# Optimization experiments

Measured on AMD Instinct MI355X. Metric: run time of the kernel, lower is better.

## Reference

```python
import jax, jax.numpy as jnp
import numpy as np
from jax import lax

WINDOW_SIZE = 11
SIGMA = 1.5
IMG_RANGE = 2.0
MS_WEIGHTS = np.array([0.0448, 0.2856, 0.3001, 0.2363, 0.1333], dtype=np.float32)


def _gauss_window(k=WINDOW_SIZE, sigma=SIGMA):
    x = np.arange(k, dtype=np.float64) - k // 2
    g = np.exp(-(x ** 2) / (2.0 * sigma ** 2))
    g = g / g.sum()
    return jnp.asarray(np.outer(g, g), dtype=jnp.float32)  # [k, k]


def _dwconv(x, win):
    # depthwise valid conv, groups = channels (torch conv2d weight [C,1,k,k])
    c = x.shape[1]
    k = win.shape[0]
    rhs = jnp.broadcast_to(win[None, None], (c, 1, k, k))
    return lax.conv_general_dilated(
        x, rhs, window_strides=(1, 1), padding='VALID',
        dimension_numbers=('NCHW', 'OIHW', 'NCHW'), feature_group_count=c)


def _ssim(img1, img2, win, img_range):
    mu1 = _dwconv(img1, win)
    mu2 = _dwconv(img2, win)
    mu1_sq, mu2_sq, mu1_mu2 = mu1 * mu1, mu2 * mu2, mu1 * mu2
    sigma1_sq = _dwconv(img1 * img1, win) - mu1_sq
    sigma2_sq = _dwconv(img2 * img2, win) - mu2_sq
    sigma12 = _dwconv(img1 * img2, win) - mu1_mu2
    C1 = (0.01 * img_range) ** 2
    C2 = (0.03 * img_range) ** 2
    v1 = 2.0 * sigma12 + C2
    v2 = sigma1_sq + sigma2_sq + C2
    cs = jnp.mean(v1 / v2)
    ssim_map = (2.0 * mu1_mu2 + C1) * v1 / ((mu1_sq + mu2_sq + C1) * v2)
    return jnp.mean(ssim_map), cs


def _avg_pool2(x):
    b, c, h, w = x.shape
    return x.reshape(b, c, h // 2, 2, w // 2, 2).mean(axis=(3, 5))


def _msssim_loss(img1, img2):
    win = _gauss_window()
    weights = jnp.asarray(MS_WEIGHTS)
    sims = []
    mcs = None
    for _ in range(len(MS_WEIGHTS)):  # fixed 5 pyramid levels
        sim, mcs = _ssim(img1, img2, win, IMG_RANGE)
        sims.append(sim)
        img1 = _avg_pool2(img1)
        img2 = _avg_pool2(img2)
    ssims = jnp.stack(sims)
    # faithful to source: cs from LAST level powered by weights[-1]
    output = mcs ** weights[-1] * jnp.prod(ssims ** weights)
    return 1.0 - output


def setup_inputs() -> dict:
    key = jax.random.key(0)
    k1, k2 = jax.random.split(key)
    img1 = jax.random.normal(k1, (16, 3, 512, 512), dtype=jnp.float32)
    # correlated pair so per-level SSIM/CS means stay positive (fractional powers)
    img2 = img1 + 0.05 * jax.random.normal(k2, (16, 3, 512, 512), dtype=jnp.float32)
    return {'img1': img1, 'img2': img2}


def reference(img1, img2):
    return _msssim_loss(img1, img2)
```

## Files before the change

### kernel.cpp

```cpp
#include <hip/hip_runtime.h>
#include <math.h>

#define TS 32
#define HW 42
#define SPAD 44
#define VPAD 45

#define NB0 12288
#define NB1 3072
#define NB2 768
#define NB3 192
#define NB4 48
#define NPART 16368

__global__ void msssim_init_kernel(float* __restrict__ g) {
    if (threadIdx.x == 0) {
        double w[11]; double s = 0.0;
        for (int i = 0; i < 11; ++i) { double x = (double)(i - 5); w[i] = exp(-(x * x) / 4.5); s += w[i]; }
        for (int i = 0; i < 11; ++i) g[i] = (float)(w[i] / s);
    }
}

__device__ __forceinline__ float4 prodf(float2 ab) {
    return make_float4(ab.x, ab.y, fmaf(ab.x, ab.x, ab.y * ab.y), ab.x * ab.y);
}

template<int I>
__device__ __forceinline__ float4 conv11(const float4 (&w)[11], const float (&g)[11]) {
    const float4& w0 = w[I % 11];
    float4 r;
    r.x = w0.x * g[0]; r.y = w0.y * g[0]; r.z = w0.z * g[0]; r.w = w0.w * g[0];
#pragma unroll
    for (int k = 1; k < 11; ++k) {
        const float4& wk = w[(I + k) % 11];
        r.x = fmaf(g[k], wk.x, r.x);
        r.y = fmaf(g[k], wk.y, r.y);
        r.z = fmaf(g[k], wk.z, r.z);
        r.w = fmaf(g[k], wk.w, r.w);
    }
    return r;
}

__global__ __launch_bounds__(256, 6) void ssim_fused_kernel(
    const float* __restrict__ img1, const float* __restrict__ img2,
    int H, const float* __restrict__ gg,
    float2* __restrict__ partials,
    float* __restrict__ o1, float* __restrict__ o2)
{
    __shared__ __align__(16) float2 sAB[HW][SPAD];
    __shared__ __align__(16) float4 vrt[16][VPAD];
    __shared__ float gsh[11];
    __shared__ float red[8];

    const int tid = threadIdx.x;
    if (tid < 11) gsh[tid] = gg[tid];

    const int W = H, Hv = H - 10, Wv = W - 10;
    const int bx = blockIdx.x * TS, by = blockIdx.y * TS;
    const size_t plane = (size_t)blockIdx.z * (size_t)H * (size_t)W;
    const float* __restrict__ p1 = img1 + plane;
    const float* __restrict__ p2 = img2 + plane;

    for (int i = tid; i < HW * 21; i += 256) {
        int r = i / 21, j = i - r * 21, cc = 2 * j;
        int y = by + r, x = bx + cc;
        float2 a = make_float2(0.f, 0.f), b = a;
        if (y < H && x + 1 < W) {
            size_t o = (size_t)y * W + x;
            a = *(const float2*)(p1 + o);
            b = *(const float2*)(p2 + o);
        }
        *(float4*)&sAB[r][cc] = make_float4(a.x, b.x, a.y, b.y);
    }
    __syncthreads();

    float g[11];
#pragma unroll
    for (int j = 0; j < 11; ++j) g[j] = gsh[j];

    if (o1) {
        int py = tid >> 4, px = tid & 15;
        float4 q0 = *(const float4*)&sAB[2 * py][2 * px];
        float4 q1 = *(const float4*)&sAB[2 * py + 1][2 * px];
        int Hp = H >> 1;
        size_t po = (size_t)blockIdx.z * Hp * Hp + (size_t)((by >> 1) + py) * Hp + (bx >> 1) + px;
        o1[po] = 0.25f * ((q0.x + q0.z) + (q1.x + q1.z));
        o2[po] = 0.25f * ((q0.y + q0.w) + (q1.y + q1.w));
    }

    const int cvert = tid % 42, chv = tid / 42;
    const int r0v = (chv < 4) ? 3 * chv : 12 + 2 * (chv - 4);
    const int lenv = (chv < 4) ? 3 : 2;

    const float C1 = 0.0004f;
    const float C2 = 0.0036f;
    float ssim_l = 0.f, cs_l = 0.f;

#pragma unroll
    for (int p = 0; p < 2; ++p) {
        if (p) __syncthreads();

        if (tid < 252) {
            const int base = 16 * p + r0v;
            float4 w[11];
#pragma unroll
            for (int j = 0; j < 10; ++j) w[j] = prodf(sAB[base + j][cvert]);
#define P1STEP(I)                                                      \
            if ((I) < 2 || lenv == 3) {                                \
                w[(10 + (I)) % 11] = prodf(sAB[base + 10 + (I)][cvert]); \
                vrt[r0v + (I)][cvert] = conv11<(I)>(w, g);             \
            }
            P1STEP(0) P1STEP(1) P1STEP(2)
#undef P1STEP
        }
        __syncthreads();

        {
            const int row = tid >> 4, c0 = (tid & 15) * 2;
            const int oy = by + 16 * p + row;
            float4 w[11];
#pragma unroll
            for (int j = 0; j < 10; ++j) w[j] = vrt[row][c0 + j];
#define P2STEP(I)                                                      \
            {                                                          \
                w[(10 + (I)) % 11] = vrt[row][c0 + 10 + (I)];          \
                float4 m = conv11<(I)>(w, g);                          \
                int ox = bx + c0 + (I);                                \
                if (oy < Hv && ox < Wv) {                              \
                    float ab   = m.x * m.y;                            \
                    float aabb = fmaf(m.x, m.x, m.y * m.y);            \
                    float n1   = fmaf(2.f, ab, C1);                    \
                    float d1   = aabb + C1;                            \
                    float v1   = fmaf(2.f, m.w - ab, C2);              \
                    float v2   = (m.z - aabb) + C2;                    \
                    float rden = 1.f / (d1 * v2);                      \
                    cs_l   = fmaf(v1 * d1, rden, cs_l);                \
                    ssim_l = fmaf(n1 * v1, rden, ssim_l);              \
                }                                                      \
            }
            P2STEP(0) P2STEP(1)
#undef P2STEP
        }
    }

#pragma unroll
    for (int off = 32; off > 0; off >>= 1) {
        ssim_l += __shfl_down(ssim_l, off);
        cs_l   += __shfl_down(cs_l, off);
    }
    int wave = tid >> 6, lane = tid & 63;
    if (lane == 0) { red[wave] = ssim_l; red[4 + wave] = cs_l; }
    __syncthreads();
    if (tid == 0) {
        float ss = red[0] + red[1] + red[2] + red[3];
        float cc = red[4] + red[5] + red[6] + red[7];
        int nt = gridDim.x;
        int bid = ((int)blockIdx.z * nt + (int)blockIdx.y) * nt + (int)blockIdx.x;
        partials[bid] = make_float2(ss, cc);
    }
}

__global__ __launch_bounds__(1024) void msssim_reduce_kernel(
    const float2* __restrict__ partials, float* __restrict__ out)
{
    __shared__ double sred[16][2];
    __shared__ double lev[10];
    const int NB[5]  = {NB0, NB1, NB2, NB3, NB4};
    const int OFF[5] = {0, NB0, NB0 + NB1, NB0 + NB1 + NB2, NB0 + NB1 + NB2 + NB3};
    const int tid = threadIdx.x;
    const int wv = tid >> 6, ln = tid & 63;

    for (int l = 0; l < 5; ++l) {
        double s = 0.0, c = 0.0;
        for (int i = tid; i < NB[l]; i += 1024) {
            float2 p = partials[OFF[l] + i];
            s += (double)p.x; c += (double)p.y;
        }
#pragma unroll
        for (int off = 32; off > 0; off >>= 1) {
            s += __shfl_down(s, off);
            c += __shfl_down(c, off);
        }
        if (ln == 0) { sred[wv][0] = s; sred[wv][1] = c; }
        __syncthreads();
        if (tid == 0) {
            double ss = 0.0, cc = 0.0;
            for (int w = 0; w < 16; ++w) { ss += sred[w][0]; cc += sred[w][1]; }
            lev[l] = ss; lev[5 + l] = cc;
        }
        __syncthreads();
    }

    if (tid == 0) {
        const double counts[5] = {
            48.0 * 502.0 * 502.0,
            48.0 * 246.0 * 246.0,
            48.0 * 118.0 * 118.0,
            48.0 * 54.0 * 54.0,
            48.0 * 22.0 * 22.0
        };
        const double w[5] = { (double)0.0448f, (double)0.2856f, (double)0.3001f,
                              (double)0.2363f, (double)0.1333f };
        double prod = 1.0;
        for (int i = 0; i < 5; ++i) prod *= pow(lev[i] / counts[i], w[i]);
        double mcs = lev[9] / counts[4];
        double output = pow(mcs, w[4]) * prod;
        out[0] = (float)(1.0 - output);
    }
}

extern "C" void kernel_launch(void* const* d_in, const int* in_sizes, int n_in,
                              void* d_out, int out_size, void* d_ws, size_t ws_size,
                              hipStream_t stream) {
    const float* img1 = (const float*)d_in[0];
    const float* img2 = (const float*)d_in[1];
    float* out = (float*)d_out;

    char* ws = (char*)d_ws;
    float* g = (float*)ws;
    float2* partials = (float2*)(ws + 256);
    float* buf = (float*)(ws + 256 + NPART * sizeof(float2));

    const int NC = 48;
    const int Hs[5] = {512, 256, 128, 64, 32};

    const float* A[5]; const float* B[5];
    float* Aw[5]; float* Bw[5];
    A[0] = img1; B[0] = img2;
    Aw[0] = Bw[0] = nullptr;
    size_t o = 0;
    for (int l = 1; l < 5; ++l) {
        size_t n = (size_t)NC * Hs[l] * Hs[l];
        Aw[l] = buf + o; o += n;
        Bw[l] = buf + o; o += n;
        A[l] = Aw[l]; B[l] = Bw[l];
    }

    const int OFF[5] = {0, NB0, NB0 + NB1, NB0 + NB1 + NB2, NB0 + NB1 + NB2 + NB3};

    msssim_init_kernel<<<dim3(1), dim3(64), 0, stream>>>(g);

    for (int l = 0; l < 5; ++l) {
        int H = Hs[l];
        int nt = H / TS;
        dim3 grid(nt, nt, NC);
        float* po1 = (l < 4) ? Aw[l + 1] : nullptr;
        float* po2 = (l < 4) ? Bw[l + 1] : nullptr;
        ssim_fused_kernel<<<grid, dim3(256), 0, stream>>>(
            A[l], B[l], H, g, partials + OFF[l], po1, po2);
    }

    msssim_reduce_kernel<<<dim3(1), dim3(1024), 0, stream>>>(partials, out);
}
```

Measured before the change: 221.4 us.

## Merge pyramid levels 1-4 into one launch and restructure separable conv

Levels 1-4 now run in a single kernel launch. Each level's input is rebuilt on the fly by recursive average-pooling of the level-1 buffer instead of materializing every level, which removes three launches and the intermediate writes. The separable Gaussian conv is reworked so each thread accumulates four outputs as packed float2 FMAs from paired rows in shared memory. It also switches to a fast reciprocal. In exchange, deep levels re-read many level-1 pixels per output, and fewer threads are active in each conv phase.

```diff
diff --git a/kernel.cpp b/kernel.cpp
--- a/kernel.cpp
+++ b/kernel.cpp
@@ -1,10 +1,7 @@
 #include <hip/hip_runtime.h>
 #include <math.h>
 
-#define TS 32
-#define HW 42
-#define SPAD 44
-#define VPAD 45
+typedef float vf2 __attribute__((ext_vector_type(2)));
 
 #define NB0 12288
 #define NB1 3072
@@ -21,125 +18,168 @@
     }
 }
 
-__device__ __forceinline__ float4 prodf(float2 ab) {
-    return make_float4(ab.x, ab.y, fmaf(ab.x, ab.x, ab.y * ab.y), ab.x * ab.y);
-}
-
-template<int I>
-__device__ __forceinline__ float4 conv11(const float4 (&w)[11], const float (&g)[11]) {
-    const float4& w0 = w[I % 11];
-    float4 r;
-    r.x = w0.x * g[0]; r.y = w0.y * g[0]; r.z = w0.z * g[0]; r.w = w0.w * g[0];
-#pragma unroll
-    for (int k = 1; k < 11; ++k) {
-        const float4& wk = w[(I + k) % 11];
-        r.x = fmaf(g[k], wk.x, r.x);
-        r.y = fmaf(g[k], wk.y, r.y);
-        r.z = fmaf(g[k], wk.z, r.z);
-        r.w = fmaf(g[k], wk.w, r.w);
-    }
-    return r;
-}
-
-__global__ __launch_bounds__(256, 6) void ssim_fused_kernel(
-    const float* __restrict__ img1, const float* __restrict__ img2,
-    int H, const float* __restrict__ gg,
-    float2* __restrict__ partials,
+struct Smem {
+    float4 sAB2[21][43];
+    float4 vrt[16][45];
+    float red[8];
+};
+
+template<int F>
+__device__ __forceinline__ float poolrec(const float* __restrict__ p, int Y, int X) {
+    if constexpr (F == 2) {
+        float2 r0 = *(const float2*)(p + (size_t)Y * 256 + X);
+        float2 r1 = *(const float2*)(p + (size_t)(Y + 1) * 256 + X);
+        return 0.25f * ((r0.x + r0.y) + (r1.x + r1.y));
+    } else {
+        constexpr int H = F / 2;
+        return 0.25f * ((poolrec<H>(p, Y, X) + poolrec<H>(p, Y, X + H))
+                      + (poolrec<H>(p, Y + H, X) + poolrec<H>(p, Y + H, X + H)));
+    }
+}
+
+template<int J>
+__device__ __forceinline__ void vtap(vf2 m, const float (&g)[11], vf2 (&amu)[4], vf2 (&aq)[4]) {
+    vf2 t = m * m;
+    vf2 q = { t.x + t.y, m.x * m.y };
+#pragma unroll
+    for (int i = 0; i < 4; ++i) {
+        if (J - i >= 0 && J - i <= 10) {
+            vf2 gs = { g[J - i], g[J - i] };
+            amu[i] = __builtin_elementwise_fma(gs, m, amu[i]);
+            aq[i]  = __builtin_elementwise_fma(gs, q, aq[i]);
+        }
+    }
+}
+
+template<int T>
+__device__ __forceinline__ void htap(const float4 V, const float (&g)[11], vf2 (&amu)[4], vf2 (&aq)[4]) {
+    vf2 mt = { V.x, V.y }, qt = { V.z, V.w };
+#pragma unroll
+    for (int i = 0; i < 4; ++i) {
+        if (T - i >= 0 && T - i <= 10) {
+            vf2 gs = { g[T - i], g[T - i] };
+            amu[i] = __builtin_elementwise_fma(gs, mt, amu[i]);
+            aq[i]  = __builtin_elementwise_fma(gs, qt, aq[i]);
+        }
+    }
+}
+
+template<int L>
+__device__ __forceinline__ void ssim_body(Smem& sm, int tbx, int tby, int z,
+    const float* __restrict__ i1, const float* __restrict__ i2,
+    const float* __restrict__ gg, float2* __restrict__ partials, int pidx,
     float* __restrict__ o1, float* __restrict__ o2)
 {
-    __shared__ __align__(16) float2 sAB[HW][SPAD];
-    __shared__ __align__(16) float4 vrt[16][VPAD];
-    __shared__ float gsh[11];
-    __shared__ float red[8];
-
+    constexpr int Hl = 512 >> L;
+    constexpr int Hv = Hl - 10;
     const int tid = threadIdx.x;
-    if (tid < 11) gsh[tid] = gg[tid];
-
-    const int W = H, Hv = H - 10, Wv = W - 10;
-    const int bx = blockIdx.x * TS, by = blockIdx.y * TS;
-    const size_t plane = (size_t)blockIdx.z * (size_t)H * (size_t)W;
-    const float* __restrict__ p1 = img1 + plane;
-    const float* __restrict__ p2 = img2 + plane;
-
-    for (int i = tid; i < HW * 21; i += 256) {
-        int r = i / 21, j = i - r * 21, cc = 2 * j;
-        int y = by + r, x = bx + cc;
-        float2 a = make_float2(0.f, 0.f), b = a;
-        if (y < H && x + 1 < W) {
-            size_t o = (size_t)y * W + x;
-            a = *(const float2*)(p1 + o);
-            b = *(const float2*)(p2 + o);
-        }
-        *(float4*)&sAB[r][cc] = make_float4(a.x, b.x, a.y, b.y);
+    const int bx = tbx * 32, by = tby * 32;
+
+    float g[11];
+#pragma unroll
+    for (int j = 0; j < 11; ++j) g[j] = gg[j];
+
+    if constexpr (L <= 1) {
+        const float* p1 = i1 + (size_t)z * Hl * Hl;
+        const float* p2 = i2 + (size_t)z * Hl * Hl;
+        for (int i = tid; i < 441; i += 256) {
+            int rp = i / 21, cp = i - rp * 21, c = 2 * cp;
+            int y = by + 2 * rp, x = bx + c;
+            float2 a0 = {0.f,0.f}, a1 = a0, b0 = a0, b1 = a0;
+            if (y < Hl && x < Hl) {
+                const float* r1p = p1 + (size_t)y * Hl + x;
+                a0 = *(const float2*)r1p;
+                a1 = *(const float2*)(r1p + Hl);
+                const float* r2p = p2 + (size_t)y * Hl + x;
+                b0 = *(const float2*)r2p;
+                b1 = *(const float2*)(r2p + Hl);
+            }
+            sm.sAB2[rp][c]     = make_float4(a0.x, b0.x, a1.x, b1.x);
+            sm.sAB2[rp][c + 1] = make_float4(a0.y, b0.y, a1.y, b1.y);
+        }
+    } else {
+        constexpr int F = 1 << (L - 1);
+        const float* p1 = i1 + (size_t)z * 65536;
+        const float* p2 = i2 + (size_t)z * 65536;
+        for (int i = tid; i < 441; i += 256) {
+            int rp = i / 21, cp = i - rp * 21, c = 2 * cp;
+            int ly = by + 2 * rp, lx = bx + c;
+            float a00=0.f,a01=0.f,a10=0.f,a11=0.f,b00=0.f,b01=0.f,b10=0.f,b11=0.f;
+            if (ly < Hl && lx < Hl) {
+                int Y = ly * F, X = lx * F;
+                a00 = poolrec<F>(p1, Y, X);         b00 = poolrec<F>(p2, Y, X);
+                a01 = poolrec<F>(p1, Y, X + F);     b01 = poolrec<F>(p2, Y, X + F);
+                a10 = poolrec<F>(p1, Y + F, X);     b10 = poolrec<F>(p2, Y + F, X);
+                a11 = poolrec<F>(p1, Y + F, X + F); b11 = poolrec<F>(p2, Y + F, X + F);
+            }
+            sm.sAB2[rp][c]     = make_float4(a00, b00, a10, b10);
+            sm.sAB2[rp][c + 1] = make_float4(a01, b01, a11, b11);
+        }
     }
     __syncthreads();
 
-    float g[11];
-#pragma unroll
-    for (int j = 0; j < 11; ++j) g[j] = gsh[j];
-
-    if (o1) {
+    if constexpr (L == 0) {
         int py = tid >> 4, px = tid & 15;
-        float4 q0 = *(const float4*)&sAB[2 * py][2 * px];
-        float4 q1 = *(const float4*)&sAB[2 * py + 1][2 * px];
-        int Hp = H >> 1;
-        size_t po = (size_t)blockIdx.z * Hp * Hp + (size_t)((by >> 1) + py) * Hp + (bx >> 1) + px;
-        o1[po] = 0.25f * ((q0.x + q0.z) + (q1.x + q1.z));
-        o2[po] = 0.25f * ((q0.y + q0.w) + (q1.y + q1.w));
-    }
-
-    const int cvert = tid % 42, chv = tid / 42;
-    const int r0v = (chv < 4) ? 3 * chv : 12 + 2 * (chv - 4);
-    const int lenv = (chv < 4) ? 3 : 2;
-
-    const float C1 = 0.0004f;
-    const float C2 = 0.0036f;
+        float4 q0 = sm.sAB2[py][2 * px];
+        float4 q1 = sm.sAB2[py][2 * px + 1];
+        size_t po = (size_t)z * 65536 + (size_t)(tby * 16 + py) * 256 + (tbx * 16 + px);
+        o1[po] = 0.25f * ((q0.x + q1.x) + (q0.z + q1.z));
+        o2[po] = 0.25f * ((q0.y + q1.y) + (q0.w + q1.w));
+    }
+
     float ssim_l = 0.f, cs_l = 0.f;
 
 #pragma unroll
     for (int p = 0; p < 2; ++p) {
         if (p) __syncthreads();
 
-        if (tid < 252) {
-            const int base = 16 * p + r0v;
-            float4 w[11];
-#pragma unroll
-            for (int j = 0; j < 10; ++j) w[j] = prodf(sAB[base + j][cvert]);
-#define P1STEP(I)                                                      \
-            if ((I) < 2 || lenv == 3) {                                \
-                w[(10 + (I)) % 11] = prodf(sAB[base + 10 + (I)][cvert]); \
-                vrt[r0v + (I)][cvert] = conv11<(I)>(w, g);             \
+        if (tid < 168) {
+            int c = tid % 42, ch = tid / 42;
+            int rp0 = 8 * p + 2 * ch;
+            vf2 amu[4], aq[4];
+#pragma unroll
+            for (int i = 0; i < 4; ++i) { amu[i] = (vf2){0.f,0.f}; aq[i] = (vf2){0.f,0.f}; }
+#define VPAIR(K) { float4 Q = sm.sAB2[rp0 + (K)][c];                  \
+                   vtap<2*(K)>((vf2){Q.x, Q.y}, g, amu, aq);          \
+                   vtap<2*(K)+1>((vf2){Q.z, Q.w}, g, amu, aq); }
+            VPAIR(0) VPAIR(1) VPAIR(2) VPAIR(3) VPAIR(4) VPAIR(5) VPAIR(6)
+#undef VPAIR
+            int r0 = 4 * ch;
+#pragma unroll
+            for (int i = 0; i < 4; ++i)
+                sm.vrt[r0 + i][c] = make_float4(amu[i].x, amu[i].y, aq[i].x, aq[i].y);
+        }
+        __syncthreads();
+
+        if (tid < 128) {
+            int row = tid >> 3, oct = tid & 7, c0 = 4 * oct;
+            int oy = by + 16 * p + row;
+            vf2 amu[4], aq[4];
+#pragma unroll
+            for (int i = 0; i < 4; ++i) { amu[i] = (vf2){0.f,0.f}; aq[i] = (vf2){0.f,0.f}; }
+#define HT(T) htap<(T)>(sm.vrt[row][c0 + (T)], g, amu, aq);
+            HT(0) HT(1) HT(2) HT(3) HT(4) HT(5) HT(6)
+            HT(7) HT(8) HT(9) HT(10) HT(11) HT(12) HT(13)
+#undef HT
+            if (oy < Hv) {
+#pragma unroll
+                for (int i = 0; i < 4; ++i) {
+                    int ox = bx + c0 + i;
+                    if (ox < Hv) {
+                        vf2 mu = amu[i], qq = aq[i];
+                        float ab = mu.x * mu.y;
+                        vf2 t = mu * mu;
+                        float aabb = t.x + t.y;
+                        float n1 = fmaf(2.f, ab, 0.0004f);
+                        float d1 = aabb + 0.0004f;
+                        float v1 = fmaf(2.f, qq.y - ab, 0.0036f);
+                        float v2 = (qq.x - aabb) + 0.0036f;
+                        float rden = __builtin_amdgcn_rcpf(d1 * v2);
+                        cs_l   = fmaf(v1 * d1, rden, cs_l);
+                        ssim_l = fmaf(n1 * v1, rden, ssim_l);
+                    }
+                }
             }
-            P1STEP(0) P1STEP(1) P1STEP(2)
-#undef P1STEP
-        }
-        __syncthreads();
-
-        {
-            const int row = tid >> 4, c0 = (tid & 15) * 2;
-            const int oy = by + 16 * p + row;
-            float4 w[11];
-#pragma unroll
-            for (int j = 0; j < 10; ++j) w[j] = vrt[row][c0 + j];
-#define P2STEP(I)                                                      \
-            {                                                          \
-                w[(10 + (I)) % 11] = vrt[row][c0 + 10 + (I)];          \
-                float4 m = conv11<(I)>(w, g);                          \
-                int ox = bx + c0 + (I);                                \
-                if (oy < Hv && ox < Wv) {                              \
-                    float ab   = m.x * m.y;                            \
-                    float aabb = fmaf(m.x, m.x, m.y * m.y);            \
-                    float n1   = fmaf(2.f, ab, C1);                    \
-                    float d1   = aabb + C1;                            \
-                    float v1   = fmaf(2.f, m.w - ab, C2);              \
-                    float v2   = (m.z - aabb) + C2;                    \
-                    float rden = 1.f / (d1 * v2);                      \
-                    cs_l   = fmaf(v1 * d1, rden, cs_l);                \
-                    ssim_l = fmaf(n1 * v1, rden, ssim_l);              \
-                }                                                      \
-            }
-            P2STEP(0) P2STEP(1)
-#undef P2STEP
         }
     }
 
@@ -149,14 +189,43 @@
         cs_l   += __shfl_down(cs_l, off);
     }
     int wave = tid >> 6, lane = tid & 63;
-    if (lane == 0) { red[wave] = ssim_l; red[4 + wave] = cs_l; }
+    if (lane == 0) { sm.red[wave] = ssim_l; sm.red[4 + wave] = cs_l; }
     __syncthreads();
     if (tid == 0) {
-        float ss = red[0] + red[1] + red[2] + red[3];
-        float cc = red[4] + red[5] + red[6] + red[7];
-        int nt = gridDim.x;
-        int bid = ((int)blockIdx.z * nt + (int)blockIdx.y) * nt + (int)blockIdx.x;
-        partials[bid] = make_float2(ss, cc);
+        float ss = sm.red[0] + sm.red[1] + sm.red[2] + sm.red[3];
+        float cc = sm.red[4] + sm.red[5] + sm.red[6] + sm.red[7];
+        partials[pidx] = make_float2(ss, cc);
+    }
+}
+
+__global__ __launch_bounds__(256, 6) void ssim_l0_kernel(
+    const float* __restrict__ img1, const float* __restrict__ img2,
+    const float* __restrict__ gg, float2* __restrict__ partials,
+    float* __restrict__ o1, float* __restrict__ o2)
+{
+    __shared__ Smem sm;
+    int pidx = ((int)blockIdx.z * 16 + (int)blockIdx.y) * 16 + (int)blockIdx.x;
+    ssim_body<0>(sm, blockIdx.x, blockIdx.y, blockIdx.z, img1, img2, gg, partials, pidx, o1, o2);
+}
+
+__global__ __launch_bounds__(256, 6) void ssim_rest_kernel(
+    const float* __restrict__ L1a, const float* __restrict__ L1b,
+    const float* __restrict__ gg, float2* __restrict__ partials)
+{
+    __shared__ Smem sm;
+    int b = blockIdx.x;
+    if (b < 3072) {
+        int lb = b;        int z = lb >> 6; int r = lb & 63; int tby = r >> 3; int tbx = r & 7;
+        ssim_body<1>(sm, tbx, tby, z, L1a, L1b, gg, partials, 12288 + lb, nullptr, nullptr);
+    } else if (b < 3840) {
+        int lb = b - 3072; int z = lb >> 4; int r = lb & 15; int tby = r >> 2; int tbx = r & 3;
+        ssim_body<2>(sm, tbx, tby, z, L1a, L1b, gg, partials, 15360 + lb, nullptr, nullptr);
+    } else if (b < 4032) {
+        int lb = b - 3840; int z = lb >> 2; int r = lb & 3;  int tby = r >> 1; int tbx = r & 1;
+        ssim_body<3>(sm, tbx, tby, z, L1a, L1b, gg, partials, 16128 + lb, nullptr, nullptr);
+    } else {
+        int lb = b - 4032;
+        ssim_body<4>(sm, 0, 0, lb, L1a, L1b, gg, partials, 16320 + lb, nullptr, nullptr);
     }
 }
 
@@ -219,36 +288,15 @@
     char* ws = (char*)d_ws;
     float* g = (float*)ws;
     float2* partials = (float2*)(ws + 256);
-    float* buf = (float*)(ws + 256 + NPART * sizeof(float2));
-
-    const int NC = 48;
-    const int Hs[5] = {512, 256, 128, 64, 32};
-
-    const float* A[5]; const float* B[5];
-    float* Aw[5]; float* Bw[5];
-    A[0] = img1; B[0] = img2;
-    Aw[0] = Bw[0] = nullptr;
-    size_t o = 0;
-    for (int l = 1; l < 5; ++l) {
-        size_t n = (size_t)NC * Hs[l] * Hs[l];
-        Aw[l] = buf + o; o += n;
-        Bw[l] = buf + o; o += n;
-        A[l] = Aw[l]; B[l] = Bw[l];
-    }
-
-    const int OFF[5] = {0, NB0, NB0 + NB1, NB0 + NB1 + NB2, NB0 + NB1 + NB2 + NB3};
+    float* Aw1 = (float*)(ws + 256 + 131072);
+    float* Bw1 = Aw1 + (size_t)48 * 65536;
 
     msssim_init_kernel<<<dim3(1), dim3(64), 0, stream>>>(g);
 
-    for (int l = 0; l < 5; ++l) {
-        int H = Hs[l];
-        int nt = H / TS;
-        dim3 grid(nt, nt, NC);
-        float* po1 = (l < 4) ? Aw[l + 1] : nullptr;
-        float* po2 = (l < 4) ? Bw[l + 1] : nullptr;
-        ssim_fused_kernel<<<grid, dim3(256), 0, stream>>>(
-            A[l], B[l], H, g, partials + OFF[l], po1, po2);
-    }
+    ssim_l0_kernel<<<dim3(16, 16, 48), dim3(256), 0, stream>>>(
+        img1, img2, g, partials, Aw1, Bw1);
+
+    ssim_rest_kernel<<<dim3(4080), dim3(256), 0, stream>>>(Aw1, Bw1, g, partials);
 
     msssim_reduce_kernel<<<dim3(1), dim3(1024), 0, stream>>>(partials, out);
 }
```

New measurement: 230.5 us. 4.1% more time.
